# Kernel tuning notes

Hardware: AMD Instinct MI355X
Metric: run time of the kernel (lower is better)

## Reference

```python
import jax, jax.numpy as jnp
import numpy as np
from jax import lax

B, C, H, W = 16, 3, 256, 256
K = 3          # lbp kernel size (odd)
POOL = 2
Q = 8          # quant_len
LN_EPS = 1e-5


def _lbp_kernel(c, k):
    half = k // 2
    idx_pairs = [[[0, 0], [k - 1, k - 1]],
                 [[0, half], [k - 1, half]],
                 [[0, k - 1], [k - 1, 0]],
                 [[half, k - 1], [half, 0]]]
    kerns = []
    for pair in idx_pairs:
        for idx in pair:
            m = np.zeros((c, k, k), np.float32)
            m[:, half, half] = 1.0
            m[:, idx[0], idx[1]] = -1.0
            kerns.append(m)
    return jnp.asarray(np.stack(kerns))  # [8, C, K, K]


LBP_KERNEL = _lbp_kernel(C, K)


def setup_inputs() -> dict:
    key = jax.random.key(0)
    ks = jax.random.split(key, 8)
    return {
        "x": jax.random.normal(ks[0], (B, C, H, W), jnp.float32),
        "clamp_low": jnp.float32(-150.0),
        "clamp_high": jnp.float32(150.0),
        "w_expand": jax.random.normal(ks[1], (56, 3, 1, 1), jnp.float32) * 0.1,
        "b_expand": jax.random.normal(ks[2], (56,), jnp.float32) * 0.05,
        "w_conv": jax.random.normal(ks[3], (16, 4, 1, 1), jnp.float32) * 0.1,
        "b_conv": jax.random.normal(ks[4], (16,), jnp.float32) * 0.05,
        "w_final": jax.random.normal(ks[5], (1, 16, 3, 3), jnp.float32) * 0.1,
        "b_final": jax.random.normal(ks[6], (1,), jnp.float32) * 0.05,
    }


def reference(x, clamp_low, clamp_high, w_expand, b_expand, w_conv, b_conv, w_final, b_final):
    leaky = lambda v: jax.nn.leaky_relu(v, 0.01)
    bsz = x.shape[0]

    # avg_pool2d(kernel=POOL, stride=1, pad=POOL//2, count_include_pad=True) -> [B,C,H+1,W+1]
    pad = POOL // 2
    xp = lax.reduce_window(x, 0.0, lax.add, (1, 1, POOL, POOL), (1, 1, 1, 1),
                           [(0, 0), (0, 0), (pad, pad), (pad, pad)]) / float(POOL * POOL)

    # LBP difference conv: 8 output channels, SAME padding
    hk = K // 2
    xl = lax.conv_general_dilated(xp, LBP_KERNEL, (1, 1), [(hk, hk), (hk, hk)],
                                  dimension_numbers=("NCHW", "OIHW", "NCHW"))
    xl = jnp.clip(xl, clamp_low, clamp_high)

    b4 = bsz * 4
    hp, wp = xl.shape[-2], xl.shape[-1]
    n = hp * wp
    xl = xl.reshape(b4, 2, n)  # [B4, 2, N]

    # per-sample, per-channel quantization boundaries: measure[b,i,c] = i*cd + min
    mn = xl.min(axis=-1)                       # [B4, 2]
    mx = xl.max(axis=-1)                       # [B4, 2]
    cd = (mx - mn) / Q
    measure = jnp.arange(Q + 1, dtype=xl.dtype)[None, :, None] * cd[:, None, :] + mn[:, None, :]  # [B4,Q+1,2]

    def bin_mask(vals, ch):
        # keep raw value where lo_i <= v <= hi_i, else 0  -> [B4, Q, N]
        v = vals[:, None, :]
        lo = measure[:, :-1, ch][:, :, None]
        hi = measure[:, 1:, ch][:, :, None]
        return jnp.where((v >= lo) & (v <= hi), v, 0.0)

    m0 = bin_mask(xl[:, 0, :], 0)  # [B4, Q, N]
    m1 = bin_mask(xl[:, 1, :], 1)  # [B4, Q, N]

    # joint histogram of masked values: equivalent to per-pixel outer product + one-hot mask conv
    hist = jnp.einsum("bin,bjn->bij", m0, m1)       # [B4, Q, Q]
    hist = hist / jnp.sum(hist)                      # global normalizer (torch.sum(x))
    hist = hist.reshape(b4, Q * Q, 1)

    # levels: (bin_index + 1) * measure[:, 1, :]
    ii, jj = jnp.meshgrid(jnp.arange(Q), jnp.arange(Q), indexing="ij")
    idxs = jnp.stack([ii, jj], axis=-1).reshape(Q * Q, 2)          # cartesian_prod order
    levels = (idxs[None].astype(xl.dtype) + 1.0) * measure[:, 1, :][:, None, :]  # [B4,64,2]

    feat = jnp.concatenate([levels, hist], axis=2)   # [B4, 64, 3]
    feat = feat.reshape(bsz, 4, Q * Q, 3).transpose(0, 3, 1, 2)  # [B, 3, 4, 64]

    # 1x1 conv 3 -> 56
    h = leaky(jnp.einsum("bcij,oc->boij", feat, w_expand[:, :, 0, 0]) + b_expand[None, :, None, None])
    h = h.transpose(0, 2, 3, 1)  # [B, 4, 64, 56] -> channels=4, spatial (64,56)

    # nearest interpolate spatial (64,56) -> (H,W): src = floor(dst * in / out)
    src_h = (jnp.arange(H) * h.shape[2]) // H
    src_w = (jnp.arange(W) * h.shape[3]) // W
    h = h[:, :, src_h][:, :, :, src_w]  # [B, 4, H, W]

    # layer_norm over last two dims, no affine
    mean = h.mean(axis=(-2, -1), keepdims=True)
    var = jnp.mean((h - mean) ** 2, axis=(-2, -1), keepdims=True)
    h = (h - mean) / jnp.sqrt(var + LN_EPS)

    # 1x1 conv 4 -> 16
    h = leaky(jnp.einsum("bchw,oc->bohw", h, w_conv[:, :, 0, 0]) + b_conv[None, :, None, None])

    # 3x3 conv 16 -> 1, SAME padding
    out = lax.conv_general_dilated(h, w_final, (1, 1), [(1, 1), (1, 1)],
                                   dimension_numbers=("NCHW", "OIHW", "NCHW"))
    out = leaky(out + b_final[None, :, None, None])
    return out
```

## Files before the change

kernel.cpp:

```cpp
#include <hip/hip_runtime.h>
#include <stdint.h>
#include <math.h>

#define HH 256
#define WW 256
#define BATCH 16
#define HP 257
#define SROW 264
#define SH 259
#define SBP (SH*SROW)
#define NPIX (HP*HP)
#define TS 32
#define TH 9
#define NT (TH*TH)

__device__ __forceinline__ float leaky(float v){ return v >= 0.f ? v : 0.01f*v; }

__device__ __forceinline__ void group_off(int k, int& dh, int& dw){
    dh = (k == 3) ? 0 : -1;
    dw = (k == 3) ? 1 : (k - 1);
}

__global__ __launch_bounds__(256) void k12(const float* __restrict__ x, float* __restrict__ s,
                                           float* __restrict__ pmn, float* __restrict__ pmx,
                                           float* __restrict__ hist){
    __shared__ float xs[35][36];
    __shared__ float sh[34][35];
    __shared__ float redmn[4][8], redmx[4][8];
    int blk = blockIdx.x, tid = threadIdx.x;
    int wv = tid >> 6, lane = tid & 63;
    int b = blk / NT, tile = blk % NT;
    int ty = tile / TH, tx = tile % TH;

    if (blk == 0){
        for (int t = tid; t < 4096; t += 256) hist[t] = 0.f;
    }
    if (blk < BATCH){
        float* sb = s + (size_t)blk*SBP;
        for (int t = tid; t < 2*SROW; t += 256){
            int rr = (t < SROW) ? 0 : 258; int cc = t % SROW;
            sb[rr*SROW + cc] = 0.f;
        }
        for (int t = tid; t < 257*7; t += 256){
            int rr = 1 + t/7, k = t%7;
            int cc = (k == 0) ? 0 : (257 + k);
            sb[rr*SROW + cc] = 0.f;
        }
    }

    const float* xb = x + (size_t)b*3*HH*WW;
    int xr0 = ty*TS - 2, xc0 = tx*TS - 2;
    for (int t = tid; t < 35*35; t += 256){
        int i = t/35, j = t - i*35;
        int r = xr0 + i, c = xc0 + j;
        float v = 0.f;
        if ((unsigned)r < (unsigned)HH && (unsigned)c < (unsigned)WW){
            int o = r*WW + c;
            v = xb[o] + xb[HH*WW + o] + xb[2*HH*WW + o];
        }
        xs[i][j] = v;
    }
    __syncthreads();

    for (int t = tid; t < 34*34; t += 256){
        int i = t/34, j = t - i*34;
        int h = ty*TS - 1 + i, w = tx*TS - 1 + j;
        float v = 0.f;
        if ((unsigned)h < (unsigned)HP && (unsigned)w < (unsigned)HP)
            v = 0.25f*(xs[i][j] + xs[i][j+1] + xs[i+1][j] + xs[i+1][j+1]);
        sh[i][j] = v;
    }
    __syncthreads();

    float mn[8], mx[8];
    #pragma unroll
    for (int q=0;q<8;q++){ mn[q]=INFINITY; mx[q]=-INFINITY; }
    float* sb = s + (size_t)b*SBP;
    #pragma unroll
    for (int q4=0; q4<4; ++q4){
        int p = q4*256 + tid;
        int lr = p >> 5, lc = p & 31;
        int h = ty*TS + lr, w = tx*TS + lc;
        if (h < HP && w < HP){
            float c = sh[lr+1][lc+1];
            sb[(h+1)*SROW + (w+1)] = c;
            float d;
            d = c - sh[lr  ][lc  ]; mn[0]=fminf(mn[0],d); mx[0]=fmaxf(mx[0],d);
            d = c - sh[lr+2][lc+2]; mn[1]=fminf(mn[1],d); mx[1]=fmaxf(mx[1],d);
            d = c - sh[lr  ][lc+1]; mn[2]=fminf(mn[2],d); mx[2]=fmaxf(mx[2],d);
            d = c - sh[lr+2][lc+1]; mn[3]=fminf(mn[3],d); mx[3]=fmaxf(mx[3],d);
            d = c - sh[lr  ][lc+2]; mn[4]=fminf(mn[4],d); mx[4]=fmaxf(mx[4],d);
            d = c - sh[lr+2][lc  ]; mn[5]=fminf(mn[5],d); mx[5]=fmaxf(mx[5],d);
            d = c - sh[lr+1][lc+2]; mn[6]=fminf(mn[6],d); mx[6]=fmaxf(mx[6],d);
            d = c - sh[lr+1][lc  ]; mn[7]=fminf(mn[7],d); mx[7]=fmaxf(mx[7],d);
        }
    }
    #pragma unroll
    for (int off=32; off; off>>=1){
        #pragma unroll
        for (int q=0;q<8;q++){
            mn[q] = fminf(mn[q], __shfl_down(mn[q], off));
            mx[q] = fmaxf(mx[q], __shfl_down(mx[q], off));
        }
    }
    if (lane == 0){
        #pragma unroll
        for (int q=0;q<8;q++){ redmn[wv][q]=mn[q]; redmx[wv][q]=mx[q]; }
    }
    __syncthreads();
    if (tid < 8){
        pmn[(size_t)blk*8 + tid] = fminf(fminf(redmn[0][tid],redmn[1][tid]),
                                         fminf(redmn[2][tid],redmn[3][tid]));
        pmx[(size_t)blk*8 + tid] = fmaxf(fmaxf(redmx[0][tid],redmx[1][tid]),
                                         fmaxf(redmx[2][tid],redmx[3][tid]));
    }
}

__global__ __launch_bounds__(256) void k3_hist(const float* __restrict__ s, const float* __restrict__ cl,
                                               const float* __restrict__ chp,
                                               const float* __restrict__ pmn, const float* __restrict__ pmx,
                                               float* __restrict__ hist){
    __shared__ float lh[4*64*32];
    __shared__ float band[7][260];
    int bx = blockIdx.x, b = blockIdx.y;
    int tid = threadIdx.x;
    int wv = tid >> 6, lane = tid & 63;
    int h0 = bx*4;
    int nr = (bx == 63) ? 5 : 4;

    for (int t = tid; t < 4*64*32; t += 256) lh[t] = 0.f;

    const float* sb = s + (size_t)b*SBP;
    int total = (nr+2)*259;
    for (int t = tid; t < total; t += 256){
        int lr = t/259, wc = t - lr*259;
        band[lr][wc] = sb[(size_t)(h0+lr)*SROW + wc];
    }

    float mnA=INFINITY, mxA=-INFINITY, mnB=INFINITY, mxB=-INFINITY;
    for (int t = lane; t < NT; t += 64){
        const float* pn = pmn + ((size_t)(b*NT + t))*8;
        const float* px = pmx + ((size_t)(b*NT + t))*8;
        mnA = fminf(mnA, pn[2*wv]);   mxA = fmaxf(mxA, px[2*wv]);
        mnB = fminf(mnB, pn[2*wv+1]); mxB = fmaxf(mxB, px[2*wv+1]);
    }
    #pragma unroll
    for (int off=32; off; off>>=1){
        mnA = fminf(mnA, __shfl_down(mnA, off)); mxA = fmaxf(mxA, __shfl_down(mxA, off));
        mnB = fminf(mnB, __shfl_down(mnB, off)); mxB = fmaxf(mxB, __shfl_down(mxB, off));
    }
    mnA = __shfl(mnA, 0); mxA = __shfl(mxA, 0);
    mnB = __shfl(mnB, 0); mxB = __shfl(mxB, 0);
    float lo = cl[0], hi = chp[0];
    float mn0 = fminf(fmaxf(mnA, lo), hi), mx0 = fminf(fmaxf(mxA, lo), hi);
    float mn1 = fminf(fmaxf(mnB, lo), hi), mx1 = fminf(fmaxf(mxB, lo), hi);
    float cd0 = (mx0-mn0)*0.125f;
    float cd1 = (mx1-mn1)*0.125f;
    float m0[9], m1[9];
    #pragma unroll
    for (int i=0;i<9;i++){
        m0[i] = __fadd_rn(__fmul_rn((float)i, cd0), mn0);
        m1[i] = __fadd_rn(__fmul_rn((float)i, cd1), mn1);
    }
    int g = b*4 + wv;
    int dh, dw; group_off(wv, dh, dw);
    float* lhg = lh + wv*2048 + (lane & 31);
    __syncthreads();

    int npx = nr*257;
    for (int p = lane; p < npx; p += 64){
        int lrr = p/257;
        int w = p - lrr*257;
        float c = band[lrr+1][w+1];
        float v0 = fminf(fmaxf(c - band[lrr+1+dh][w+1+dw], lo), hi);
        float v1 = fminf(fmaxf(c - band[lrr+1-dh][w+1-dw], lo), hi);
        unsigned b0=0, b1=0;
        #pragma unroll
        for (int i=0;i<8;i++){
            b0 |= (v0>=m0[i] && v0<=m0[i+1]) ? (1u<<i) : 0u;
            b1 |= (v1>=m1[i] && v1<=m1[i+1]) ? (1u<<i) : 0u;
        }
        float pr = v0*v1;
        unsigned bb0=b0;
        while (bb0){
            int i = __ffs(bb0)-1; bb0 &= bb0-1;
            unsigned bb1=b1;
            while (bb1){
                int j = __ffs(bb1)-1; bb1 &= bb1-1;
                atomicAdd(&lhg[(i*8+j)*32], pr);
            }
        }
    }
    __syncthreads();
    float acc = 0.f;
    #pragma unroll
    for (int r=0;r<32;r++) acc += lh[(wv*64 + lane)*32 + ((lane + r)&31)];
    if (acc != 0.f) atomicAdd(&hist[g*64 + lane], acc);
}

__global__ __launch_bounds__(256) void k45f(const float* __restrict__ hist,
                    const float* __restrict__ pmn, const float* __restrict__ pmx,
                    const float* __restrict__ cl, const float* __restrict__ chp,
                    const float* __restrict__ we, const float* __restrict__ be,
                    const float* __restrict__ wc, const float* __restrict__ bc,
                    const float* __restrict__ wf, const float* __restrict__ bf,
                    float* __restrict__ out){
    __shared__ float hloc[4*3584];
    __shared__ float w9l[4*9*56];
    __shared__ float wfl[144];
    __shared__ float wred[4][16];
    __shared__ float gmn[8], gmx[8];
    __shared__ float gstat[8];
    __shared__ float sred[4];
    int ch = blockIdx.x, b = blockIdx.y;
    int tid = threadIdx.x;
    int wv = tid >> 6, lane = tid & 63;
    if (tid < 144) wfl[tid] = wf[tid];

    float rmn[8], rmx[8];
    #pragma unroll
    for (int q=0;q<8;q++){ rmn[q]=INFINITY; rmx[q]=-INFINITY; }
    for (int t = tid; t < NT; t += 256){
        const float* pn = pmn + ((size_t)(b*NT + t))*8;
        const float* px = pmx + ((size_t)(b*NT + t))*8;
        #pragma unroll
        for (int q=0;q<8;q++){ rmn[q]=fminf(rmn[q],pn[q]); rmx[q]=fmaxf(rmx[q],px[q]); }
    }
    #pragma unroll
    for (int off=32; off; off>>=1){
        #pragma unroll
        for (int q=0;q<8;q++){
            rmn[q] = fminf(rmn[q], __shfl_down(rmn[q], off));
            rmx[q] = fmaxf(rmx[q], __shfl_down(rmx[q], off));
        }
    }
    if (lane == 0){
        #pragma unroll
        for (int q=0;q<8;q++){ wred[wv][q]=rmn[q]; wred[wv][8+q]=rmx[q]; }
    }
    __syncthreads();
    if (tid < 8)
        gmn[tid] = fminf(fminf(wred[0][tid],wred[1][tid]), fminf(wred[2][tid],wred[3][tid]));
    else if (tid < 16){
        int q = tid-8;
        gmx[q] = fmaxf(fmaxf(wred[0][8+q],wred[1][8+q]), fmaxf(wred[2][8+q],wred[3][8+q]));
    }

    float ps = 0.f;
    for (int t = tid; t < 4096; t += 256) ps += hist[t];
    #pragma unroll
    for (int off=32; off; off>>=1) ps += __shfl_down(ps, off);
    if (lane == 0) sred[wv] = ps;
    __syncthreads();
    float S = sred[0]+sred[1]+sred[2]+sred[3];

    int g = b*4 + wv;
    float lo = cl[0], hi = chp[0];
    float mn0 = fminf(fmaxf(gmn[2*wv  ], lo), hi), mx0 = fminf(fmaxf(gmx[2*wv  ], lo), hi);
    float mn1 = fminf(fmaxf(gmn[2*wv+1], lo), hi), mx1 = fminf(fmaxf(gmx[2*wv+1], lo), hi);
    float lvl0 = __fadd_rn(__fmul_rn(1.0f,(mx0-mn0)*0.125f), mn0);
    float lvl1 = __fadd_rn(__fmul_rn(1.0f,(mx1-mn1)*0.125f), mn1);
    for (int e = lane; e < 3584; e += 64){
        int ij = e/56, o = e - ij*56;
        int i = ij>>3, j = ij&7;
        float f0 = __fmul_rn((float)(i+1), lvl0);
        float f1 = __fmul_rn((float)(j+1), lvl1);
        float f2 = hist[g*64+ij] / S;
        float a = f0*we[o*3+0] + f1*we[o*3+1] + f2*we[o*3+2] + be[o];
        hloc[wv*3584 + e] = leaky(a);
    }
    float pm = 0.f;
    for (int e = lane; e < 3584; e += 64){
        int o = e%56;
        int lo_ = (32*o+6)/7, hi_ = (32*o+31)/7;
        pm += hloc[wv*3584+e] * (float)(4*(hi_-lo_+1));
    }
    #pragma unroll
    for (int off=32; off; off>>=1) pm += __shfl_down(pm, off);
    pm = __shfl(pm, 0);
    float mean = pm * (1.0f/65536.0f);
    float pv = 0.f;
    for (int e = lane; e < 3584; e += 64){
        int o = e%56;
        int lo_ = (32*o+6)/7, hi_ = (32*o+31)/7;
        float d = hloc[wv*3584+e] - mean;
        pv += d*d * (float)(4*(hi_-lo_+1));
    }
    #pragma unroll
    for (int off=32; off; off>>=1) pv += __shfl_down(pv, off);
    pv = __shfl(pv, 0);
    if (lane == 0){
        gstat[wv*2+0] = mean;
        gstat[wv*2+1] = 1.0f / sqrtf(pv * (1.0f/65536.0f) + 1e-5f);
    }
    __syncthreads();

    int rm = (2*ch-1 > 0) ? (2*ch-1) : 0;
    int rp = (2*ch+2 < 63) ? (2*ch+2) : 63;
    int ne = (rp-rm+1)*56;
    for (int e = tid; e < ne; e += 256){
        int rr = e/56, sxc = e - rr*56;
        int eg = (rm+rr)*56 + sxc;
        float hn[4];
        #pragma unroll
        for (int k=0;k<4;k++) hn[k] = (hloc[k*3584+eg] - gstat[2*k]) * gstat[2*k+1];
        float w9v[9] = {0,0,0,0,0,0,0,0,0};
        #pragma unroll
        for (int c=0;c<16;c++){
            float hv = bc[c];
            #pragma unroll
            for (int k=0;k<4;k++) hv += wc[c*4+k]*hn[k];
            hv = leaky(hv);
            #pragma unroll
            for (int t=0;t<9;t++) w9v[t] += wfl[c*9+t]*hv;
        }
        #pragma unroll
        for (int t=0;t<9;t++) w9l[rr*504 + t*56 + sxc] = w9v[t];
    }
    __syncthreads();

    float bf0 = bf[0];
    int x = tid;
    int sxm = ((x-1)*7) >> 5;
    int sx0 = (x*7) >> 5;
    int sxp = ((x+1)*7) >> 5;
    for (int yo=0; yo<8; ++yo){
        int y = ch*8 + yo;
        float acc = bf0;
        #pragma unroll
        for (int dy=0; dy<3; ++dy){
            int yy = y + dy - 1;
            if ((unsigned)yy >= 256u) continue;
            const float* wr = &w9l[((yy>>2) - rm)*504 + dy*3*56];
            if (x >= 1)   acc += wr[sxm];
                          acc += wr[56 + sx0];
            if (x <= 254) acc += wr[2*56 + sxp];
        }
        out[((size_t)(b*256 + y))*256 + x] = leaky(acc);
    }
}

extern "C" void kernel_launch(void* const* d_in, const int* in_sizes, int n_in,
                              void* d_out, int out_size, void* d_ws, size_t ws_size,
                              hipStream_t stream){
    const float* x  = (const float*)d_in[0];
    const float* cl = (const float*)d_in[1];
    const float* ch = (const float*)d_in[2];
    const float* we = (const float*)d_in[3];
    const float* be = (const float*)d_in[4];
    const float* wc = (const float*)d_in[5];
    const float* bc = (const float*)d_in[6];
    const float* wf = (const float*)d_in[7];
    const float* bf = (const float*)d_in[8];
    float* out = (float*)d_out;

    float* s = (float*)d_ws;
    size_t off = (size_t)BATCH*SBP;
    float* pmn  = s + off; off += (size_t)BATCH*NT*8;
    float* pmx  = s + off; off += (size_t)BATCH*NT*8;
    float* hist = s + off; off += 4096;

    k12<<<BATCH*NT, 256, 0, stream>>>(x, s, pmn, pmx, hist);
    k3_hist<<<dim3(64,BATCH), 256, 0, stream>>>(s, cl, ch, pmn, pmx, hist);
    k45f<<<dim3(32,BATCH), 256, 0, stream>>>(hist, pmn, pmx, cl, ch, we, be, wc, bc, wf, bf, out);
}
```

Before: 158.5 us.

## Fuse three kernels into one persistent kernel with grid-wide barriers

```diff
diff --git a/kernel.cpp b/kernel.cpp
--- a/kernel.cpp
+++ b/kernel.cpp
@@ -9,10 +9,17 @@
 #define SROW 264
 #define SH 259
 #define SBP (SH*SROW)
-#define NPIX (HP*HP)
 #define TS 32
 #define TH 9
 #define NT (TH*TH)
+#define NTILES (BATCH*NT)
+#define NVB 512
+
+struct SA { float xs[35][36]; float sh[34][35]; float redmn[4][8]; float redmx[4][8]; };
+struct SB { float lh[4*64*32]; float band[11][260]; };
+struct SC { float hloc[4*3584]; float w9l[4*9*56]; float wfl[144]; float wred[4][16];
+            float gmn[8]; float gmx[8]; float gstat[8]; float sred[4]; };
+union  SU { SA a; SB b; SC c; };
 
 __device__ __forceinline__ float leaky(float v){ return v >= 0.f ? v : 0.01f*v; }
 
@@ -21,14 +28,28 @@
     dw = (k == 3) ? 1 : (k - 1);
 }
 
-__global__ __launch_bounds__(256) void k12(const float* __restrict__ x, float* __restrict__ s,
-                                           float* __restrict__ pmn, float* __restrict__ pmx,
-                                           float* __restrict__ hist){
-    __shared__ float xs[35][36];
-    __shared__ float sh[34][35];
-    __shared__ float redmn[4][8], redmx[4][8];
-    int blk = blockIdx.x, tid = threadIdx.x;
-    int wv = tid >> 6, lane = tid & 63;
+__device__ __forceinline__ void grid_barrier(unsigned* bar, int slot, int nblk){
+    __syncthreads();
+    if (threadIdx.x == 0){
+        __threadfence();
+        unsigned prev = __hip_atomic_fetch_add(&bar[slot*2], 1u, __ATOMIC_ACQ_REL,
+                                               __HIP_MEMORY_SCOPE_AGENT);
+        if (prev + 1u == (unsigned)nblk){
+            __hip_atomic_store(&bar[slot*2+1], 1u, __ATOMIC_RELEASE, __HIP_MEMORY_SCOPE_AGENT);
+        } else {
+            while (__hip_atomic_load(&bar[slot*2+1], __ATOMIC_ACQUIRE,
+                                     __HIP_MEMORY_SCOPE_AGENT) == 0u)
+                __builtin_amdgcn_s_sleep(2);
+        }
+        __threadfence();
+    }
+    __syncthreads();
+}
+
+__device__ void phaseA_tile(SA& A, int blk, const float* __restrict__ x, float* __restrict__ s,
+                            float* __restrict__ pmn, float* __restrict__ pmx, float* __restrict__ hist)
+{
+    int tid = threadIdx.x, wv = tid >> 6, lane = tid & 63;
     int b = blk / NT, tile = blk % NT;
     int ty = tile / TH, tx = tile % TH;
 
@@ -58,7 +79,7 @@
             int o = r*WW + c;
             v = xb[o] + xb[HH*WW + o] + xb[2*HH*WW + o];
         }
-        xs[i][j] = v;
+        A.xs[i][j] = v;
     }
     __syncthreads();
 
@@ -67,8 +88,8 @@
         int h = ty*TS - 1 + i, w = tx*TS - 1 + j;
         float v = 0.f;
         if ((unsigned)h < (unsigned)HP && (unsigned)w < (unsigned)HP)
-            v = 0.25f*(xs[i][j] + xs[i][j+1] + xs[i+1][j] + xs[i+1][j+1]);
-        sh[i][j] = v;
+            v = 0.25f*(A.xs[i][j] + A.xs[i][j+1] + A.xs[i+1][j] + A.xs[i+1][j+1]);
+        A.sh[i][j] = v;
     }
     __syncthreads();
 
@@ -82,17 +103,17 @@
         int lr = p >> 5, lc = p & 31;
         int h = ty*TS + lr, w = tx*TS + lc;
         if (h < HP && w < HP){
-            float c = sh[lr+1][lc+1];
+            float c = A.sh[lr+1][lc+1];
             sb[(h+1)*SROW + (w+1)] = c;
             float d;
-            d = c - sh[lr  ][lc  ]; mn[0]=fminf(mn[0],d); mx[0]=fmaxf(mx[0],d);
-            d = c - sh[lr+2][lc+2]; mn[1]=fminf(mn[1],d); mx[1]=fmaxf(mx[1],d);
-            d = c - sh[lr  ][lc+1]; mn[2]=fminf(mn[2],d); mx[2]=fmaxf(mx[2],d);
-            d = c - sh[lr+2][lc+1]; mn[3]=fminf(mn[3],d); mx[3]=fmaxf(mx[3],d);
-            d = c - sh[lr  ][lc+2]; mn[4]=fminf(mn[4],d); mx[4]=fmaxf(mx[4],d);
-            d = c - sh[lr+2][lc  ]; mn[5]=fminf(mn[5],d); mx[5]=fmaxf(mx[5],d);
-            d = c - sh[lr+1][lc+2]; mn[6]=fminf(mn[6],d); mx[6]=fmaxf(mx[6],d);
-            d = c - sh[lr+1][lc  ]; mn[7]=fminf(mn[7],d); mx[7]=fmaxf(mx[7],d);
+            d = c - A.sh[lr  ][lc  ]; mn[0]=fminf(mn[0],d); mx[0]=fmaxf(mx[0],d);
+            d = c - A.sh[lr+2][lc+2]; mn[1]=fminf(mn[1],d); mx[1]=fmaxf(mx[1],d);
+            d = c - A.sh[lr  ][lc+1]; mn[2]=fminf(mn[2],d); mx[2]=fmaxf(mx[2],d);
+            d = c - A.sh[lr+2][lc+1]; mn[3]=fminf(mn[3],d); mx[3]=fmaxf(mx[3],d);
+            d = c - A.sh[lr  ][lc+2]; mn[4]=fminf(mn[4],d); mx[4]=fmaxf(mx[4],d);
+            d = c - A.sh[lr+2][lc  ]; mn[5]=fminf(mn[5],d); mx[5]=fmaxf(mx[5],d);
+            d = c - A.sh[lr+1][lc+2]; mn[6]=fminf(mn[6],d); mx[6]=fmaxf(mx[6],d);
+            d = c - A.sh[lr+1][lc  ]; mn[7]=fminf(mn[7],d); mx[7]=fmaxf(mx[7],d);
         }
     }
     #pragma unroll
@@ -105,36 +126,34 @@
     }
     if (lane == 0){
         #pragma unroll
-        for (int q=0;q<8;q++){ redmn[wv][q]=mn[q]; redmx[wv][q]=mx[q]; }
+        for (int q=0;q<8;q++){ A.redmn[wv][q]=mn[q]; A.redmx[wv][q]=mx[q]; }
     }
     __syncthreads();
     if (tid < 8){
-        pmn[(size_t)blk*8 + tid] = fminf(fminf(redmn[0][tid],redmn[1][tid]),
-                                         fminf(redmn[2][tid],redmn[3][tid]));
-        pmx[(size_t)blk*8 + tid] = fmaxf(fmaxf(redmx[0][tid],redmx[1][tid]),
-                                         fmaxf(redmx[2][tid],redmx[3][tid]));
-    }
-}
-
-__global__ __launch_bounds__(256) void k3_hist(const float* __restrict__ s, const float* __restrict__ cl,
-                                               const float* __restrict__ chp,
-                                               const float* __restrict__ pmn, const float* __restrict__ pmx,
-                                               float* __restrict__ hist){
-    __shared__ float lh[4*64*32];
-    __shared__ float band[7][260];
-    int bx = blockIdx.x, b = blockIdx.y;
-    int tid = threadIdx.x;
-    int wv = tid >> 6, lane = tid & 63;
-    int h0 = bx*4;
-    int nr = (bx == 63) ? 5 : 4;
-
-    for (int t = tid; t < 4*64*32; t += 256) lh[t] = 0.f;
+        pmn[(size_t)blk*8 + tid] = fminf(fminf(A.redmn[0][tid],A.redmn[1][tid]),
+                                         fminf(A.redmn[2][tid],A.redmn[3][tid]));
+        pmx[(size_t)blk*8 + tid] = fmaxf(fmaxf(A.redmx[0][tid],A.redmx[1][tid]),
+                                         fmaxf(A.redmx[2][tid],A.redmx[3][tid]));
+    }
+}
+
+__device__ void phaseB_band(SB& Bm, int vb, const float* __restrict__ s, const float* __restrict__ cl,
+                            const float* __restrict__ chp,
+                            const float* __restrict__ pmn, const float* __restrict__ pmx,
+                            float* __restrict__ hist)
+{
+    int tid = threadIdx.x, wv = tid >> 6, lane = tid & 63;
+    int c = vb & 31, b = vb >> 5;
+    int h0 = c*8;
+    int nr = (c == 31) ? 9 : 8;
+
+    for (int t = tid; t < 4*64*32; t += 256) Bm.lh[t] = 0.f;
 
     const float* sb = s + (size_t)b*SBP;
-    int total = (nr+2)*259;
+    int total = (nr+2)*260;
     for (int t = tid; t < total; t += 256){
-        int lr = t/259, wc = t - lr*259;
-        band[lr][wc] = sb[(size_t)(h0+lr)*SROW + wc];
+        int lr = t/260, wc2 = t - lr*260;
+        Bm.band[lr][wc2] = sb[(size_t)(h0+lr)*SROW + wc2];
     }
 
     float mnA=INFINITY, mxA=-INFINITY, mnB=INFINITY, mxB=-INFINITY;
@@ -164,16 +183,16 @@
     }
     int g = b*4 + wv;
     int dh, dw; group_off(wv, dh, dw);
-    float* lhg = lh + wv*2048 + (lane & 31);
+    float* lhg = Bm.lh + wv*2048 + (lane & 31);
     __syncthreads();
 
     int npx = nr*257;
     for (int p = lane; p < npx; p += 64){
         int lrr = p/257;
         int w = p - lrr*257;
-        float c = band[lrr+1][w+1];
-        float v0 = fminf(fmaxf(c - band[lrr+1+dh][w+1+dw], lo), hi);
-        float v1 = fminf(fmaxf(c - band[lrr+1-dh][w+1-dw], lo), hi);
+        float cc = Bm.band[lrr+1][w+1];
+        float v0 = fminf(fmaxf(cc - Bm.band[lrr+1+dh][w+1+dw], lo), hi);
+        float v1 = fminf(fmaxf(cc - Bm.band[lrr+1-dh][w+1-dw], lo), hi);
         unsigned b0=0, b1=0;
         #pragma unroll
         for (int i=0;i<8;i++){
@@ -194,28 +213,21 @@
     __syncthreads();
     float acc = 0.f;
     #pragma unroll
-    for (int r=0;r<32;r++) acc += lh[(wv*64 + lane)*32 + ((lane + r)&31)];
+    for (int r=0;r<32;r++) acc += Bm.lh[(wv*64 + lane)*32 + ((lane + r)&31)];
     if (acc != 0.f) atomicAdd(&hist[g*64 + lane], acc);
 }
 
-__global__ __launch_bounds__(256) void k45f(const float* __restrict__ hist,
+__device__ void phaseC_block(SC& Cm, int vb, const float* __restrict__ hist,
                     const float* __restrict__ pmn, const float* __restrict__ pmx,
                     const float* __restrict__ cl, const float* __restrict__ chp,
                     const float* __restrict__ we, const float* __restrict__ be,
                     const float* __restrict__ wc, const float* __restrict__ bc,
                     const float* __restrict__ wf, const float* __restrict__ bf,
-                    float* __restrict__ out){
-    __shared__ float hloc[4*3584];
-    __shared__ float w9l[4*9*56];
-    __shared__ float wfl[144];
-    __shared__ float wred[4][16];
-    __shared__ float gmn[8], gmx[8];
-    __shared__ float gstat[8];
-    __shared__ float sred[4];
-    int ch = blockIdx.x, b = blockIdx.y;
-    int tid = threadIdx.x;
-    int wv = tid >> 6, lane = tid & 63;
-    if (tid < 144) wfl[tid] = wf[tid];
+                    float* __restrict__ out)
+{
+    int tid = threadIdx.x, wv = tid >> 6, lane = tid & 63;
+    int ch = vb & 31, b = vb >> 5;
+    if (tid < 144) Cm.wfl[tid] = wf[tid];
 
     float rmn[8], rmx[8];
     #pragma unroll
@@ -236,28 +248,28 @@
     }
     if (lane == 0){
         #pragma unroll
-        for (int q=0;q<8;q++){ wred[wv][q]=rmn[q]; wred[wv][8+q]=rmx[q]; }
+        for (int q=0;q<8;q++){ Cm.wred[wv][q]=rmn[q]; Cm.wred[wv][8+q]=rmx[q]; }
     }
     __syncthreads();
     if (tid < 8)
-        gmn[tid] = fminf(fminf(wred[0][tid],wred[1][tid]), fminf(wred[2][tid],wred[3][tid]));
+        Cm.gmn[tid] = fminf(fminf(Cm.wred[0][tid],Cm.wred[1][tid]), fminf(Cm.wred[2][tid],Cm.wred[3][tid]));
     else if (tid < 16){
         int q = tid-8;
-        gmx[q] = fmaxf(fmaxf(wred[0][8+q],wred[1][8+q]), fmaxf(wred[2][8+q],wred[3][8+q]));
+        Cm.gmx[q] = fmaxf(fmaxf(Cm.wred[0][8+q],Cm.wred[1][8+q]), fmaxf(Cm.wred[2][8+q],Cm.wred[3][8+q]));
     }
 
     float ps = 0.f;
     for (int t = tid; t < 4096; t += 256) ps += hist[t];
     #pragma unroll
     for (int off=32; off; off>>=1) ps += __shfl_down(ps, off);
-    if (lane == 0) sred[wv] = ps;
-    __syncthreads();
-    float S = sred[0]+sred[1]+sred[2]+sred[3];
+    if (lane == 0) Cm.sred[wv] = ps;
+    __syncthreads();
+    float S = Cm.sred[0]+Cm.sred[1]+Cm.sred[2]+Cm.sred[3];
 
     int g = b*4 + wv;
     float lo = cl[0], hi = chp[0];
-    float mn0 = fminf(fmaxf(gmn[2*wv  ], lo), hi), mx0 = fminf(fmaxf(gmx[2*wv  ], lo), hi);
-    float mn1 = fminf(fmaxf(gmn[2*wv+1], lo), hi), mx1 = fminf(fmaxf(gmx[2*wv+1], lo), hi);
+    float mn0 = fminf(fmaxf(Cm.gmn[2*wv  ], lo), hi), mx0 = fminf(fmaxf(Cm.gmx[2*wv  ], lo), hi);
+    float mn1 = fminf(fmaxf(Cm.gmn[2*wv+1], lo), hi), mx1 = fminf(fmaxf(Cm.gmx[2*wv+1], lo), hi);
     float lvl0 = __fadd_rn(__fmul_rn(1.0f,(mx0-mn0)*0.125f), mn0);
     float lvl1 = __fadd_rn(__fmul_rn(1.0f,(mx1-mn1)*0.125f), mn1);
     for (int e = lane; e < 3584; e += 64){
@@ -267,13 +279,13 @@
         float f1 = __fmul_rn((float)(j+1), lvl1);
         float f2 = hist[g*64+ij] / S;
         float a = f0*we[o*3+0] + f1*we[o*3+1] + f2*we[o*3+2] + be[o];
-        hloc[wv*3584 + e] = leaky(a);
+        Cm.hloc[wv*3584 + e] = leaky(a);
     }
     float pm = 0.f;
     for (int e = lane; e < 3584; e += 64){
         int o = e%56;
         int lo_ = (32*o+6)/7, hi_ = (32*o+31)/7;
-        pm += hloc[wv*3584+e] * (float)(4*(hi_-lo_+1));
+        pm += Cm.hloc[wv*3584+e] * (float)(4*(hi_-lo_+1));
     }
     #pragma unroll
     for (int off=32; off; off>>=1) pm += __shfl_down(pm, off);
@@ -283,15 +295,15 @@
     for (int e = lane; e < 3584; e += 64){
         int o = e%56;
         int lo_ = (32*o+6)/7, hi_ = (32*o+31)/7;
-        float d = hloc[wv*3584+e] - mean;
+        float d = Cm.hloc[wv*3584+e] - mean;
         pv += d*d * (float)(4*(hi_-lo_+1));
     }
     #pragma unroll
     for (int off=32; off; off>>=1) pv += __shfl_down(pv, off);
     pv = __shfl(pv, 0);
     if (lane == 0){
-        gstat[wv*2+0] = mean;
-        gstat[wv*2+1] = 1.0f / sqrtf(pv * (1.0f/65536.0f) + 1e-5f);
+        Cm.gstat[wv*2+0] = mean;
+        Cm.gstat[wv*2+1] = 1.0f / sqrtf(pv * (1.0f/65536.0f) + 1e-5f);
     }
     __syncthreads();
 
@@ -303,19 +315,19 @@
         int eg = (rm+rr)*56 + sxc;
         float hn[4];
         #pragma unroll
-        for (int k=0;k<4;k++) hn[k] = (hloc[k*3584+eg] - gstat[2*k]) * gstat[2*k+1];
+        for (int k=0;k<4;k++) hn[k] = (Cm.hloc[k*3584+eg] - Cm.gstat[2*k]) * Cm.gstat[2*k+1];
         float w9v[9] = {0,0,0,0,0,0,0,0,0};
         #pragma unroll
-        for (int c=0;c<16;c++){
-            float hv = bc[c];
+        for (int c2=0;c2<16;c2++){
+            float hv = bc[c2];
             #pragma unroll
-            for (int k=0;k<4;k++) hv += wc[c*4+k]*hn[k];
+            for (int k=0;k<4;k++) hv += wc[c2*4+k]*hn[k];
             hv = leaky(hv);
             #pragma unroll
-            for (int t=0;t<9;t++) w9v[t] += wfl[c*9+t]*hv;
-        }
-        #pragma unroll
-        for (int t=0;t<9;t++) w9l[rr*504 + t*56 + sxc] = w9v[t];
+            for (int t=0;t<9;t++) w9v[t] += Cm.wfl[c2*9+t]*hv;
+        }
+        #pragma unroll
+        for (int t=0;t<9;t++) Cm.w9l[rr*504 + t*56 + sxc] = w9v[t];
     }
     __syncthreads();
 
@@ -331,12 +343,42 @@
         for (int dy=0; dy<3; ++dy){
             int yy = y + dy - 1;
             if ((unsigned)yy >= 256u) continue;
-            const float* wr = &w9l[((yy>>2) - rm)*504 + dy*3*56];
+            const float* wr = &Cm.w9l[((yy>>2) - rm)*504 + dy*3*56];
             if (x >= 1)   acc += wr[sxm];
                           acc += wr[56 + sx0];
             if (x <= 254) acc += wr[2*56 + sxp];
         }
         out[((size_t)(b*256 + y))*256 + x] = leaky(acc);
+    }
+}
+
+__global__ __launch_bounds__(256, 2) void fused(int nblk, unsigned* __restrict__ bar,
+                    const float* __restrict__ x, float* __restrict__ s,
+                    float* __restrict__ pmn, float* __restrict__ pmx, float* __restrict__ hist,
+                    const float* __restrict__ cl, const float* __restrict__ chp,
+                    const float* __restrict__ we, const float* __restrict__ be,
+                    const float* __restrict__ wc, const float* __restrict__ bc,
+                    const float* __restrict__ wf, const float* __restrict__ bf,
+                    float* __restrict__ out)
+{
+    __shared__ SU sm;
+    int bid = blockIdx.x;
+
+    for (int blk = bid; blk < NTILES; blk += nblk){
+        __syncthreads();
+        phaseA_tile(sm.a, blk, x, s, pmn, pmx, hist);
+    }
+    grid_barrier(bar, 0, nblk);
+
+    for (int vb = bid; vb < NVB; vb += nblk){
+        __syncthreads();
+        phaseB_band(sm.b, vb, s, cl, chp, pmn, pmx, hist);
+    }
+    grid_barrier(bar, 1, nblk);
+
+    for (int vb = bid; vb < NVB; vb += nblk){
+        __syncthreads();
+        phaseC_block(sm.c, vb, hist, pmn, pmx, cl, chp, we, be, wc, bc, wf, bf, out);
     }
 }
 
@@ -359,8 +401,13 @@
     float* pmn  = s + off; off += (size_t)BATCH*NT*8;
     float* pmx  = s + off; off += (size_t)BATCH*NT*8;
     float* hist = s + off; off += 4096;
-
-    k12<<<BATCH*NT, 256, 0, stream>>>(x, s, pmn, pmx, hist);
-    k3_hist<<<dim3(64,BATCH), 256, 0, stream>>>(s, cl, ch, pmn, pmx, hist);
-    k45f<<<dim3(32,BATCH), 256, 0, stream>>>(hist, pmn, pmx, cl, ch, we, be, wc, bc, wf, bf, out);
-}
+    unsigned* bar = (unsigned*)(s + off); off += 16;
+
+    int perCU = 0;
+    hipError_t qe = hipOccupancyMaxActiveBlocksPerMultiprocessor(&perCU, fused, 256, 0);
+    int nblk = (qe == hipSuccess && perCU >= 2) ? 512 : 256;
+
+    hipMemsetAsync(bar, 0, 4*sizeof(unsigned), stream);
+    fused<<<nblk, 256, 0, stream>>>(nblk, bar, x, s, pmn, pmx, hist,
+                                    cl, ch, we, be, wc, bc, wf, bf, out);
+}
```

Measured after the change: 264.3 us. 66.8% more time.

## Retile pooling kernel into full-width row bands with float4 loads and padded layout

Applied to the files above, without the earlier changes.

```diff
diff --git a/kernel.cpp b/kernel.cpp
--- a/kernel.cpp
+++ b/kernel.cpp
@@ -9,10 +9,8 @@
 #define SROW 264
 #define SH 259
 #define SBP (SH*SROW)
-#define NPIX (HP*HP)
-#define TS 32
-#define TH 9
-#define NT (TH*TH)
+#define NPART 32
+
 
 __device__ __forceinline__ float leaky(float v){ return v >= 0.f ? v : 0.01f*v; }
 
@@ -21,79 +19,81 @@
     dw = (k == 3) ? 1 : (k - 1);
 }
 
-__global__ __launch_bounds__(256) void k12(const float* __restrict__ x, float* __restrict__ s,
-                                           float* __restrict__ pmn, float* __restrict__ pmx,
-                                           float* __restrict__ hist){
-    __shared__ float xs[35][36];
-    __shared__ float sh[34][35];
+__global__ __launch_bounds__(256) void k1(const float* __restrict__ x, float* __restrict__ s,
+                                          float* __restrict__ pmn, float* __restrict__ pmx,
+                                          float* __restrict__ hist){
+    __shared__ __align__(16) float xs[12][264];
+    __shared__ __align__(16) float ps[11][264];
     __shared__ float redmn[4][8], redmx[4][8];
-    int blk = blockIdx.x, tid = threadIdx.x;
-    int wv = tid >> 6, lane = tid & 63;
-    int b = blk / NT, tile = blk % NT;
-    int ty = tile / TH, tx = tile % TH;
-
-    if (blk == 0){
+    int c = blockIdx.x, b = blockIdx.y;
+    int tid = threadIdx.x, wv = tid >> 6, lane = tid & 63;
+    int h0 = c*8;
+    int nr = (c == 31) ? 9 : 8;
+
+    if (c == 0 && b == 0){
         for (int t = tid; t < 4096; t += 256) hist[t] = 0.f;
     }
-    if (blk < BATCH){
-        float* sb = s + (size_t)blk*SBP;
-        for (int t = tid; t < 2*SROW; t += 256){
-            int rr = (t < SROW) ? 0 : 258; int cc = t % SROW;
-            sb[rr*SROW + cc] = 0.f;
-        }
-        for (int t = tid; t < 257*7; t += 256){
-            int rr = 1 + t/7, k = t%7;
-            int cc = (k == 0) ? 0 : (257 + k);
-            sb[rr*SROW + cc] = 0.f;
-        }
-    }
+    float* sb = s + (size_t)b*SBP;
+    for (int t = tid; t < nr*7; t += 256){
+        int rr = t/7, k = t%7;
+        int col = (k < 4) ? k : (257 + k);
+        sb[(size_t)(h0+1+rr)*SROW + col] = 0.f;
+    }
+    if (c == 0){  for (int t = tid; t < SROW; t += 256) sb[t] = 0.f; }
+    if (c == 31){ for (int t = tid; t < SROW; t += 256) sb[(size_t)258*SROW + t] = 0.f; }
 
     const float* xb = x + (size_t)b*3*HH*WW;
-    int xr0 = ty*TS - 2, xc0 = tx*TS - 2;
-    for (int t = tid; t < 35*35; t += 256){
-        int i = t/35, j = t - i*35;
-        int r = xr0 + i, c = xc0 + j;
+    for (int t = tid; t < 12*66; t += 256){
+        int i = t/66, q = t - i*66;
+        int r = h0 - 2 + i;
+        float4 v = make_float4(0.f, 0.f, 0.f, 0.f);
+        if (q >= 1 && q <= 64 && (unsigned)r < 256u){
+            const float* base = xb + (size_t)r*WW + (q-1)*4;
+            float4 a = *(const float4*)(base);
+            float4 d = *(const float4*)(base + HH*WW);
+            float4 e = *(const float4*)(base + 2*HH*WW);
+            v.x = a.x + d.x + e.x;
+            v.y = a.y + d.y + e.y;
+            v.z = a.z + d.z + e.z;
+            v.w = a.w + d.w + e.w;
+        }
+        *(float4*)&xs[i][q*4] = v;
+    }
+    __syncthreads();
+
+    int np = (nr+2)*257;
+    for (int t = tid; t < np; t += 256){
+        int j = t/257, w = t - j*257;
+        int h = h0 - 1 + j;
         float v = 0.f;
-        if ((unsigned)r < (unsigned)HH && (unsigned)c < (unsigned)WW){
-            int o = r*WW + c;
-            v = xb[o] + xb[HH*WW + o] + xb[2*HH*WW + o];
-        }
-        xs[i][j] = v;
-    }
-    __syncthreads();
-
-    for (int t = tid; t < 34*34; t += 256){
-        int i = t/34, j = t - i*34;
-        int h = ty*TS - 1 + i, w = tx*TS - 1 + j;
-        float v = 0.f;
-        if ((unsigned)h < (unsigned)HP && (unsigned)w < (unsigned)HP)
-            v = 0.25f*(xs[i][j] + xs[i][j+1] + xs[i+1][j] + xs[i+1][j+1]);
-        sh[i][j] = v;
+        if ((unsigned)h < (unsigned)HP)
+            v = 0.25f*(xs[j][w+3] + xs[j][w+4] + xs[j+1][w+3] + xs[j+1][w+4]);
+        ps[j][w+4] = v;
+    }
+    for (int t = tid; t < (nr+2)*7; t += 256){
+        int j = t/7, k = t%7;
+        ps[j][(k < 4) ? k : (257 + k)] = 0.f;
     }
     __syncthreads();
 
     float mn[8], mx[8];
     #pragma unroll
     for (int q=0;q<8;q++){ mn[q]=INFINITY; mx[q]=-INFINITY; }
-    float* sb = s + (size_t)b*SBP;
-    #pragma unroll
-    for (int q4=0; q4<4; ++q4){
-        int p = q4*256 + tid;
-        int lr = p >> 5, lc = p & 31;
-        int h = ty*TS + lr, w = tx*TS + lc;
-        if (h < HP && w < HP){
-            float c = sh[lr+1][lc+1];
-            sb[(h+1)*SROW + (w+1)] = c;
-            float d;
-            d = c - sh[lr  ][lc  ]; mn[0]=fminf(mn[0],d); mx[0]=fmaxf(mx[0],d);
-            d = c - sh[lr+2][lc+2]; mn[1]=fminf(mn[1],d); mx[1]=fmaxf(mx[1],d);
-            d = c - sh[lr  ][lc+1]; mn[2]=fminf(mn[2],d); mx[2]=fmaxf(mx[2],d);
-            d = c - sh[lr+2][lc+1]; mn[3]=fminf(mn[3],d); mx[3]=fmaxf(mx[3],d);
-            d = c - sh[lr  ][lc+2]; mn[4]=fminf(mn[4],d); mx[4]=fmaxf(mx[4],d);
-            d = c - sh[lr+2][lc  ]; mn[5]=fminf(mn[5],d); mx[5]=fmaxf(mx[5],d);
-            d = c - sh[lr+1][lc+2]; mn[6]=fminf(mn[6],d); mx[6]=fmaxf(mx[6],d);
-            d = c - sh[lr+1][lc  ]; mn[7]=fminf(mn[7],d); mx[7]=fmaxf(mx[7],d);
-        }
+    int nd = nr*257;
+    for (int t = tid; t < nd; t += 256){
+        int lr = t/257, w = t - lr*257;
+        int h = h0 + lr;
+        float cv = ps[lr+1][w+4];
+        sb[(size_t)(h+1)*SROW + (w+4)] = cv;
+        float d;
+        d = cv - ps[lr  ][w+3]; mn[0]=fminf(mn[0],d); mx[0]=fmaxf(mx[0],d);
+        d = cv - ps[lr+2][w+5]; mn[1]=fminf(mn[1],d); mx[1]=fmaxf(mx[1],d);
+        d = cv - ps[lr  ][w+4]; mn[2]=fminf(mn[2],d); mx[2]=fmaxf(mx[2],d);
+        d = cv - ps[lr+2][w+4]; mn[3]=fminf(mn[3],d); mx[3]=fmaxf(mx[3],d);
+        d = cv - ps[lr  ][w+5]; mn[4]=fminf(mn[4],d); mx[4]=fmaxf(mx[4],d);
+        d = cv - ps[lr+2][w+3]; mn[5]=fminf(mn[5],d); mx[5]=fmaxf(mx[5],d);
+        d = cv - ps[lr+1][w+5]; mn[6]=fminf(mn[6],d); mx[6]=fmaxf(mx[6],d);
+        d = cv - ps[lr+1][w+3]; mn[7]=fminf(mn[7],d); mx[7]=fmaxf(mx[7],d);
     }
     #pragma unroll
     for (int off=32; off; off>>=1){
@@ -108,6 +108,7 @@
         for (int q=0;q<8;q++){ redmn[wv][q]=mn[q]; redmx[wv][q]=mx[q]; }
     }
     __syncthreads();
+    int blk = b*NPART + c;
     if (tid < 8){
         pmn[(size_t)blk*8 + tid] = fminf(fminf(redmn[0][tid],redmn[1][tid]),
                                          fminf(redmn[2][tid],redmn[3][tid]));
@@ -116,31 +117,32 @@
     }
 }
 
-__global__ __launch_bounds__(256) void k3_hist(const float* __restrict__ s, const float* __restrict__ cl,
-                                               const float* __restrict__ chp,
-                                               const float* __restrict__ pmn, const float* __restrict__ pmx,
-                                               float* __restrict__ hist){
-    __shared__ float lh[4*64*32];
-    __shared__ float band[7][260];
-    int bx = blockIdx.x, b = blockIdx.y;
-    int tid = threadIdx.x;
-    int wv = tid >> 6, lane = tid & 63;
-    int h0 = bx*4;
-    int nr = (bx == 63) ? 5 : 4;
-
-    for (int t = tid; t < 4*64*32; t += 256) lh[t] = 0.f;
+__global__ __launch_bounds__(256) void k2(const float* __restrict__ s, const float* __restrict__ cl,
+                                          const float* __restrict__ chp,
+                                          const float* __restrict__ pmn, const float* __restrict__ pmx,
+                                          float* __restrict__ hist){
+    __shared__ __align__(16) float lh[4*64*32];
+    __shared__ __align__(16) float band[7][264];
+    int c = blockIdx.x, b = blockIdx.y;
+    int tid = threadIdx.x, wv = tid >> 6, lane = tid & 63;
+    int h0 = c*4;
+    int nr = (c == 63) ? 5 : 4;
+
+    float4 z4 = make_float4(0.f,0.f,0.f,0.f);
+    float4* lhv = (float4*)lh;
+    for (int t = tid; t < 2048; t += 256) lhv[t] = z4;
 
     const float* sb = s + (size_t)b*SBP;
-    int total = (nr+2)*259;
-    for (int t = tid; t < total; t += 256){
-        int lr = t/259, wc = t - lr*259;
-        band[lr][wc] = sb[(size_t)(h0+lr)*SROW + wc];
+    int tot = (nr+2)*66;
+    for (int t = tid; t < tot; t += 256){
+        int lr = t/66, q = t - lr*66;
+        *(float4*)&band[lr][q*4] = *(const float4*)(sb + (size_t)(h0+lr)*SROW + q*4);
     }
 
     float mnA=INFINITY, mxA=-INFINITY, mnB=INFINITY, mxB=-INFINITY;
-    for (int t = lane; t < NT; t += 64){
-        const float* pn = pmn + ((size_t)(b*NT + t))*8;
-        const float* px = pmx + ((size_t)(b*NT + t))*8;
+    for (int t = lane; t < NPART; t += 64){
+        const float* pn = pmn + ((size_t)(b*NPART + t))*8;
+        const float* px = pmx + ((size_t)(b*NPART + t))*8;
         mnA = fminf(mnA, pn[2*wv]);   mxA = fmaxf(mxA, px[2*wv]);
         mnB = fminf(mnB, pn[2*wv+1]); mxB = fmaxf(mxB, px[2*wv+1]);
     }
@@ -171,9 +173,9 @@
     for (int p = lane; p < npx; p += 64){
         int lrr = p/257;
         int w = p - lrr*257;
-        float c = band[lrr+1][w+1];
-        float v0 = fminf(fmaxf(c - band[lrr+1+dh][w+1+dw], lo), hi);
-        float v1 = fminf(fmaxf(c - band[lrr+1-dh][w+1-dw], lo), hi);
+        float cc = band[lrr+1][w+4];
+        float v0 = fminf(fmaxf(cc - band[lrr+1+dh][w+4+dw], lo), hi);
+        float v1 = fminf(fmaxf(cc - band[lrr+1-dh][w+4-dw], lo), hi);
         unsigned b0=0, b1=0;
         #pragma unroll
         for (int i=0;i<8;i++){
@@ -198,7 +200,7 @@
     if (acc != 0.f) atomicAdd(&hist[g*64 + lane], acc);
 }
 
-__global__ __launch_bounds__(256) void k45f(const float* __restrict__ hist,
+__global__ __launch_bounds__(256) void k3(const float* __restrict__ hist,
                     const float* __restrict__ pmn, const float* __restrict__ pmx,
                     const float* __restrict__ cl, const float* __restrict__ chp,
                     const float* __restrict__ we, const float* __restrict__ be,
@@ -213,16 +215,15 @@
     __shared__ float gstat[8];
     __shared__ float sred[4];
     int ch = blockIdx.x, b = blockIdx.y;
-    int tid = threadIdx.x;
-    int wv = tid >> 6, lane = tid & 63;
+    int tid = threadIdx.x, wv = tid >> 6, lane = tid & 63;
     if (tid < 144) wfl[tid] = wf[tid];
 
     float rmn[8], rmx[8];
     #pragma unroll
     for (int q=0;q<8;q++){ rmn[q]=INFINITY; rmx[q]=-INFINITY; }
-    for (int t = tid; t < NT; t += 256){
-        const float* pn = pmn + ((size_t)(b*NT + t))*8;
-        const float* px = pmx + ((size_t)(b*NT + t))*8;
+    for (int t = tid; t < NPART; t += 256){
+        const float* pn = pmn + ((size_t)(b*NPART + t))*8;
+        const float* px = pmx + ((size_t)(b*NPART + t))*8;
         #pragma unroll
         for (int q=0;q<8;q++){ rmn[q]=fminf(rmn[q],pn[q]); rmx[q]=fmaxf(rmx[q],px[q]); }
     }
@@ -306,13 +307,13 @@
         for (int k=0;k<4;k++) hn[k] = (hloc[k*3584+eg] - gstat[2*k]) * gstat[2*k+1];
         float w9v[9] = {0,0,0,0,0,0,0,0,0};
         #pragma unroll
-        for (int c=0;c<16;c++){
-            float hv = bc[c];
+        for (int c2=0;c2<16;c2++){
+            float hv = bc[c2];
             #pragma unroll
-            for (int k=0;k<4;k++) hv += wc[c*4+k]*hn[k];
+            for (int k=0;k<4;k++) hv += wc[c2*4+k]*hn[k];
             hv = leaky(hv);
             #pragma unroll
-            for (int t=0;t<9;t++) w9v[t] += wfl[c*9+t]*hv;
+            for (int t=0;t<9;t++) w9v[t] += wfl[c2*9+t]*hv;
         }
         #pragma unroll
         for (int t=0;t<9;t++) w9l[rr*504 + t*56 + sxc] = w9v[t];
@@ -356,11 +357,11 @@
 
     float* s = (float*)d_ws;
     size_t off = (size_t)BATCH*SBP;
-    float* pmn  = s + off; off += (size_t)BATCH*NT*8;
-    float* pmx  = s + off; off += (size_t)BATCH*NT*8;
+    float* pmn  = s + off; off += (size_t)BATCH*NPART*8;
+    float* pmx  = s + off; off += (size_t)BATCH*NPART*8;
     float* hist = s + off; off += 4096;
 
-    k12<<<BATCH*NT, 256, 0, stream>>>(x, s, pmn, pmx, hist);
-    k3_hist<<<dim3(64,BATCH), 256, 0, stream>>>(s, cl, ch, pmn, pmx, hist);
-    k45f<<<dim3(32,BATCH), 256, 0, stream>>>(hist, pmn, pmx, cl, ch, we, be, wc, bc, wf, bf, out);
-}
+    k1<<<dim3(32,BATCH), 256, 0, stream>>>(x, s, pmn, pmx, hist);
+    k2<<<dim3(64,BATCH), 256, 0, stream>>>(s, cl, ch, pmn, pmx, hist);
+    k3<<<dim3(32,BATCH), 256, 0, stream>>>(hist, pmn, pmx, cl, ch, we, be, wc, bc, wf, bf, out);
+}
```

After: 149.0 us. 1.06x faster.
